# Kernel optimization log

Hardware: AMD Instinct MI355X
Metric: run time of the kernel (lower is better)

Reference implementation:

```python
import jax, jax.numpy as jnp
import numpy as np

N, E, H, NH = 50000, 500000, 128, 8
DH = H // NH


def _bn(x, g, b, eps=1e-5):
    # BatchNorm1d in training mode: biased batch statistics over the node dim
    mu = x.mean(0)
    var = ((x - mu) ** 2).mean(0)
    return (x - mu) * jax.lax.rsqrt(var + eps) * g + b


def setup_inputs() -> dict:
    key = jax.random.key(0)
    ks = jax.random.split(key, 16)
    W = lambda k, shape: jax.random.normal(k, shape, jnp.float32) * 0.02
    return {
        "h": jax.random.normal(ks[0], (N, H), jnp.float32),
        "eattr": jax.random.normal(ks[1], (E, H), jnp.float32),
        "src": jax.random.randint(ks[2], (E,), 0, N, jnp.int32),
        "dst": jax.random.randint(ks[3], (E,), 0, N, jnp.int32),
        "gin_w1": W(ks[4], (H, H)), "gin_b1": jnp.zeros((H,), jnp.float32),
        "gin_w2": W(ks[5], (H, H)), "gin_b2": jnp.zeros((H,), jnp.float32),
        "wq": W(ks[6], (H, H)), "bq": jnp.zeros((H,), jnp.float32),
        "wk": W(ks[7], (H, H)), "bk": jnp.zeros((H,), jnp.float32),
        "wv": W(ks[8], (H, H)), "bv": jnp.zeros((H,), jnp.float32),
        "nl_g": jnp.ones((H,), jnp.float32), "nl_b": jnp.zeros((H,), jnp.float32),
        "na_g": jnp.ones((H,), jnp.float32), "na_b": jnp.zeros((H,), jnp.float32),
        "no_g": jnp.ones((H,), jnp.float32), "no_b": jnp.zeros((H,), jnp.float32),
        "ffn1_w": W(ks[9], (2 * H, H)), "ffn1_b": jnp.zeros((2 * H,), jnp.float32),
        "ffn2_w": W(ks[10], (H, 2 * H)), "ffn2_b": jnp.zeros((H,), jnp.float32),
    }


def reference(h, eattr, src, dst, gin_w1, gin_b1, gin_w2, gin_b2,
              wq, bq, wk, bk, wv, bv, nl_g, nl_b, na_g, na_b, no_g, no_b,
              ffn1_w, ffn1_b, ffn2_w, ffn2_b):
    h_in = h

    # --- local model: GINEConv (eps=0) ---
    msg = jax.nn.relu(h[src] + eattr)                       # [E,H]
    agg = jax.ops.segment_sum(msg, dst, num_segments=N)     # [N,H]
    z = h + agg                                             # (1+eps)*h + sum
    h_local = jax.nn.relu(z @ gin_w1.T + gin_b1) @ gin_w2.T + gin_b2
    h_local = _bn(h_in + h_local, nl_g, nl_b)               # dropout=0

    # --- global attention: SparseMHA over the edge list ---
    scale = DH ** -0.5
    q = ((h @ wq.T + bq) * scale).reshape(N, NH, DH)
    k = (h @ wk.T + bk).reshape(N, NH, DH)
    v = (h @ wv.T + bv).reshape(N, NH, DH)
    s = jnp.einsum("ehd,ehd->eh", q[src], k[dst])           # per-edge scores [E,NH]
    m = jax.ops.segment_max(s, src, num_segments=N)         # row-wise max [N,NH]
    p = jnp.exp(s - m[src])
    denom = jax.ops.segment_sum(p, src, num_segments=N)     # [N,NH]
    attn = p / denom[src]                                   # sparse row softmax [E,NH]
    out = jax.ops.segment_sum(attn[:, :, None] * v[dst], src, num_segments=N)
    h_attn = out.reshape(N, H)
    h_attn = _bn(h_in + h_attn, na_g, na_b)

    # --- combine + FFN + out norm ---
    hc = h_local + h_attn
    hc = hc + (jax.nn.relu(hc @ ffn1_w.T + ffn1_b) @ ffn2_w.T + ffn2_b)
    hc = _bn(hc, no_g, no_b)
    return (hc, eattr)
```

## Files before the change

### kernel.cpp

```cpp
#include <hip/hip_runtime.h>

#define NN 50000
#define NE 500000
#define HD 128

typedef unsigned short ushort_t;
typedef __bf16 bf16x8 __attribute__((ext_vector_type(8)));
typedef float f32x4 __attribute__((ext_vector_type(4)));

static __device__ __forceinline__ unsigned short f2bf(float f) {
  unsigned int u = __float_as_uint(f);
  unsigned int r = (u + 0x7fffu + ((u >> 16) & 1u)) >> 16;
  return (unsigned short)r;
}
static __device__ __forceinline__ float2 ldbf2(const unsigned short* p) {
  unsigned int u = *reinterpret_cast<const unsigned int*>(p);
  return make_float2(__uint_as_float(u << 16), __uint_as_float(u & 0xffff0000u));
}

__global__ __launch_bounds__(256) void hist_kernel(const int* __restrict__ src, const int* __restrict__ dst,
                                                   int* __restrict__ deg_src, int* __restrict__ deg_dst, int E) {
  int e = blockIdx.x * 256 + threadIdx.x;
  if (e < E) {
    atomicAdd(&deg_dst[dst[e]], 1);
    atomicAdd(&deg_src[src[e]], 1);
  }
}

__global__ __launch_bounds__(1024) void scan_kernel(const int* __restrict__ deg_dst, const int* __restrict__ deg_src,
                                                    int* __restrict__ off_dst, int* __restrict__ cur_dst,
                                                    int* __restrict__ off_src, int* __restrict__ cur_src, int N) {
  const int* deg = blockIdx.x ? deg_src : deg_dst;
  int* off = blockIdx.x ? off_src : off_dst;
  int* cur = blockIdx.x ? cur_src : cur_dst;
  const int CH = (N + 1023) / 1024;
  int t = threadIdx.x;
  int base = t * CH;
  int sum = 0;
  for (int i = 0; i < CH; ++i) { int idx = base + i; if (idx < N) sum += deg[idx]; }
  __shared__ int ls[1024];
  ls[t] = sum;
  __syncthreads();
  for (int o = 1; o < 1024; o <<= 1) {
    int u = (t >= o) ? ls[t - o] : 0;
    __syncthreads();
    ls[t] += u;
    __syncthreads();
  }
  int run = ls[t] - sum;
  for (int i = 0; i < CH; ++i) {
    int idx = base + i;
    if (idx < N) { off[idx] = run; cur[idx] = run; run += deg[idx]; }
  }
  if (t == 1023) off[N] = ls[1023];
}

__global__ __launch_bounds__(256) void scatter_kernel(const int* __restrict__ src, const int* __restrict__ dst,
                                                      int* __restrict__ cur_src, int* __restrict__ cur_dst,
                                                      int* __restrict__ eid_src, int* __restrict__ eid_dst, int E) {
  int e = blockIdx.x * 256 + threadIdx.x;
  if (e < E) {
    int p = atomicAdd(&cur_dst[dst[e]], 1); eid_dst[p] = e;
    int q = atomicAdd(&cur_src[src[e]], 1); eid_src[q] = e;
  }
}

__global__ __launch_bounds__(256) void hconv_kernel(const float* __restrict__ h, ushort_t* __restrict__ hb, int total4) {
  int i = blockIdx.x * 256 + threadIdx.x;
  if (i >= total4) return;
  float4 v = reinterpret_cast<const float4*>(h)[i];
  ushort4 u = { f2bf(v.x), f2bf(v.y), f2bf(v.z), f2bf(v.w) };
  reinterpret_cast<ushort4*>(hb)[i] = u;
}

template <int K, int OUTC, int MODE>
__global__ __launch_bounds__(256) void gemm_kernel(const ushort_t* __restrict__ A, const float* __restrict__ W,
                                                   const float* __restrict__ bias, const float* __restrict__ resid,
                                                   void* __restrict__ out, float scale, int nrows) {
  constexpr int KP = K + 8;
  __shared__ __align__(16) ushort_t wlds[OUTC * KP];
  constexpr int NLOAD = OUTC * K / 4;
  for (int idx = threadIdx.x; idx < NLOAD; idx += 256) {
    int r = idx / (K / 4), c4 = idx % (K / 4);
    float4 wv = reinterpret_cast<const float4*>(W)[idx];
    ushort_t* d = &wlds[r * KP + c4 * 4];
    d[0] = f2bf(wv.x); d[1] = f2bf(wv.y); d[2] = f2bf(wv.z); d[3] = f2bf(wv.w);
  }
  __syncthreads();
  const int wave = threadIdx.x >> 6, lane = threadIdx.x & 63;
  const int row0 = (blockIdx.x * 4 + wave) * 16;
  if (row0 >= nrows) return;
  const int m = lane & 15, quad = lane >> 4;
  bf16x8 afrag[K / 32];
  {
    const ushort_t* ar = A + (size_t)(row0 + m) * K + quad * 8;
#pragma unroll
    for (int kk = 0; kk < K / 32; ++kk)
      afrag[kk] = *reinterpret_cast<const bf16x8*>(ar + kk * 32);
  }
  f32x4 acc[OUTC / 16] = {};
#pragma unroll
  for (int c = 0; c < OUTC / 16; ++c) {
    const ushort_t* wr = &wlds[(c * 16 + m) * KP + quad * 8];
#pragma unroll
    for (int kk = 0; kk < K / 32; ++kk) {
      bf16x8 bfrag = *reinterpret_cast<const bf16x8*>(wr + kk * 32);
      acc[c] = __builtin_amdgcn_mfma_f32_16x16x32_bf16(afrag[kk], bfrag, acc[c], 0, 0, 0);
    }
  }
#pragma unroll
  for (int c = 0; c < OUTC / 16; ++c) {
    int col = c * 16 + m;
    float bv = bias[col];
#pragma unroll
    for (int r = 0; r < 4; ++r) {
      int grow = row0 + quad * 4 + r;
      float val = (acc[c][r] + bv) * scale;
      if constexpr (MODE & 1) val = fmaxf(val, 0.0f);
      if constexpr (MODE & 2) val += resid[(size_t)grow * OUTC + col];
      if constexpr (MODE & 4) ((ushort_t*)out)[(size_t)grow * OUTC + col] = f2bf(val);
      else ((float*)out)[(size_t)grow * OUTC + col] = val;
    }
  }
}

__global__ __launch_bounds__(256) void agg_kernel(const float* __restrict__ h, const float* __restrict__ eattr,
                                                  const int* __restrict__ src, const int* __restrict__ off_dst,
                                                  const int* __restrict__ eid_dst, float* __restrict__ out_eattr,
                                                  ushort_t* __restrict__ z_bf, int N) {
  int wave = threadIdx.x >> 6, lane = threadIdx.x & 63;
  int n = blockIdx.x * 4 + wave;
  if (n >= N) return;
  int c2 = lane * 2;
  float a0 = 0.f, a1 = 0.f;
  int beg = off_dst[n], end = off_dst[n + 1];
  for (int i = beg; i < end; ++i) {
    int e = eid_dst[i];
    int s = src[e];
    float2 ea = *reinterpret_cast<const float2*>(eattr + (size_t)e * HD + c2);
    *reinterpret_cast<float2*>(out_eattr + (size_t)e * HD + c2) = ea;
    float2 hs = *reinterpret_cast<const float2*>(h + (size_t)s * HD + c2);
    a0 += fmaxf(hs.x + ea.x, 0.f);
    a1 += fmaxf(hs.y + ea.y, 0.f);
  }
  float2 hn = *reinterpret_cast<const float2*>(h + (size_t)n * HD + c2);
  ushort2 u = { f2bf(hn.x + a0), f2bf(hn.y + a1) };
  *reinterpret_cast<ushort2*>(z_bf + (size_t)n * HD + c2) = u;
}

__global__ __launch_bounds__(256) void attn_kernel(const ushort_t* __restrict__ qb, const ushort_t* __restrict__ kb,
                                                   const ushort_t* __restrict__ vb, const int* __restrict__ off_src,
                                                   const int* __restrict__ eid_src, const int* __restrict__ dst,
                                                   const float* __restrict__ h, float* __restrict__ X2, int N) {
  int wave = threadIdx.x >> 6, lane = threadIdx.x & 63;
  int n = blockIdx.x * 4 + wave;
  if (n >= N) return;
  int c2 = lane * 2;
  float2 qv = ldbf2(qb + (size_t)n * HD + c2);
  float m = -__builtin_inff(), l = 0.f, a0 = 0.f, a1 = 0.f;
  int beg = off_src[n], end = off_src[n + 1];
  for (int i = beg; i < end; ++i) {
    int e = eid_src[i];
    int d = dst[e];
    float2 kd = ldbf2(kb + (size_t)d * HD + c2);
    float s = qv.x * kd.x + qv.y * kd.y;
    s += __shfl_xor(s, 1, 64);
    s += __shfl_xor(s, 2, 64);
    s += __shfl_xor(s, 4, 64);
    float2 vd = ldbf2(vb + (size_t)d * HD + c2);
    float nm = fmaxf(m, s);
    float al = __expf(m - nm);
    float p = __expf(s - nm);
    l = l * al + p;
    a0 = a0 * al + p * vd.x;
    a1 = a1 * al + p * vd.y;
    m = nm;
  }
  float inv = (end > beg) ? 1.0f / l : 0.f;
  size_t base = (size_t)n * HD + c2;
  float2 hv = *reinterpret_cast<const float2*>(h + base);
  float2 o = make_float2(hv.x + a0 * inv, hv.y + a1 * inv);
  *reinterpret_cast<float2*>(X2 + base) = o;
}

__global__ __launch_bounds__(256) void stats_kernel(const float* __restrict__ X, float* __restrict__ sums,
                                                    float* __restrict__ sumsq, int N) {
  int col = threadIdx.x & 127, half = threadIdx.x >> 7;
  float s = 0.f, s2 = 0.f;
  for (int r = blockIdx.x * 2 + half; r < N; r += gridDim.x * 2) {
    float v = X[(size_t)r * HD + col];
    s += v;
    s2 += v * v;
  }
  __shared__ float ls[256], ls2[256];
  ls[threadIdx.x] = s;
  ls2[threadIdx.x] = s2;
  __syncthreads();
  if (half == 0) {
    s += ls[threadIdx.x + 128];
    s2 += ls2[threadIdx.x + 128];
    atomicAdd(&sums[col], s);
    atomicAdd(&sumsq[col], s2);
  }
}

__global__ void coeff_kernel(const float* __restrict__ sums, const float* __restrict__ sumsq,
                             const float* __restrict__ g, const float* __restrict__ b, float* __restrict__ ab, int N) {
  int c = threadIdx.x;
  float inv_n = 1.0f / (float)N;
  float mu = sums[c] * inv_n;
  float var = sumsq[c] * inv_n - mu * mu;
  float a = g[c] * rsqrtf(var + 1e-5f);
  ab[c] = a;
  ab[128 + c] = b[c] - mu * a;
}

__global__ __launch_bounds__(256) void combine_kernel(const float* __restrict__ X1, const float* __restrict__ X2,
                                                      const float* __restrict__ ab1, const float* __restrict__ ab2,
                                                      float* __restrict__ hc_f, ushort_t* __restrict__ hc_b, int total4) {
  int i = blockIdx.x * 256 + threadIdx.x;
  if (i >= total4) return;
  float4 x1 = reinterpret_cast<const float4*>(X1)[i];
  float4 x2 = reinterpret_cast<const float4*>(X2)[i];
  int c = (i * 4) & 127;
  float4 r;
  r.x = x1.x * ab1[c + 0] + ab1[128 + c + 0] + x2.x * ab2[c + 0] + ab2[128 + c + 0];
  r.y = x1.y * ab1[c + 1] + ab1[128 + c + 1] + x2.y * ab2[c + 1] + ab2[128 + c + 1];
  r.z = x1.z * ab1[c + 2] + ab1[128 + c + 2] + x2.z * ab2[c + 2] + ab2[128 + c + 2];
  r.w = x1.w * ab1[c + 3] + ab1[128 + c + 3] + x2.w * ab2[c + 3] + ab2[128 + c + 3];
  reinterpret_cast<float4*>(hc_f)[i] = r;
  ushort4 u = { f2bf(r.x), f2bf(r.y), f2bf(r.z), f2bf(r.w) };
  reinterpret_cast<ushort4*>(hc_b)[i] = u;
}

__global__ __launch_bounds__(256) void final_kernel(const float* __restrict__ X3, const float* __restrict__ ab,
                                                    float* __restrict__ out, int total4) {
  int i = blockIdx.x * 256 + threadIdx.x;
  if (i >= total4) return;
  float4 x = reinterpret_cast<const float4*>(X3)[i];
  int c = (i * 4) & 127;
  float4 r;
  r.x = x.x * ab[c + 0] + ab[128 + c + 0];
  r.y = x.y * ab[c + 1] + ab[128 + c + 1];
  r.z = x.z * ab[c + 2] + ab[128 + c + 2];
  r.w = x.w * ab[c + 3] + ab[128 + c + 3];
  reinterpret_cast<float4*>(out)[i] = r;
}

extern "C" void kernel_launch(void* const* d_in, const int* in_sizes, int n_in,
                              void* d_out, int out_size, void* d_ws, size_t ws_size,
                              hipStream_t stream) {
  const float* h = (const float*)d_in[0];
  const float* eattr = (const float*)d_in[1];
  const int* src = (const int*)d_in[2];
  const int* dst = (const int*)d_in[3];
  const float* gin_w1 = (const float*)d_in[4];
  const float* gin_b1 = (const float*)d_in[5];
  const float* gin_w2 = (const float*)d_in[6];
  const float* gin_b2 = (const float*)d_in[7];
  const float* wq = (const float*)d_in[8];
  const float* bq = (const float*)d_in[9];
  const float* wk = (const float*)d_in[10];
  const float* bk = (const float*)d_in[11];
  const float* wv = (const float*)d_in[12];
  const float* bv = (const float*)d_in[13];
  const float* nl_g = (const float*)d_in[14];
  const float* nl_b = (const float*)d_in[15];
  const float* na_g = (const float*)d_in[16];
  const float* na_b = (const float*)d_in[17];
  const float* no_g = (const float*)d_in[18];
  const float* no_b = (const float*)d_in[19];
  const float* ffn1_w = (const float*)d_in[20];
  const float* ffn1_b = (const float*)d_in[21];
  const float* ffn2_w = (const float*)d_in[22];
  const float* ffn2_b = (const float*)d_in[23];

  const int N = NN, E = NE;
  char* ws = (char*)d_ws;
  size_t off = 0;
  auto alloc = [&](size_t bytes) -> void* {
    void* p = ws + off;
    off += (bytes + 255) & ~(size_t)255;
    return p;
  };

  ushort_t* h_bf = (ushort_t*)alloc((size_t)N * HD * 2);
  ushort_t* q_bf = (ushort_t*)alloc((size_t)N * HD * 2);
  ushort_t* k_bf = (ushort_t*)alloc((size_t)N * HD * 2);
  ushort_t* v_bf = (ushort_t*)alloc((size_t)N * HD * 2);
  ushort_t* z_bf = (ushort_t*)alloc((size_t)N * HD * 2);
  ushort_t* mid1 = (ushort_t*)alloc((size_t)N * HD * 2);
  ushort_t* hc_bf = (ushort_t*)alloc((size_t)N * HD * 2);
  ushort_t* mid2 = (ushort_t*)alloc((size_t)N * 256 * 2);
  float* X1 = (float*)alloc((size_t)N * HD * 4);
  float* X2 = (float*)alloc((size_t)N * HD * 4);
  float* X3 = (float*)alloc((size_t)N * HD * 4);
  float* hc_f = (float*)alloc((size_t)N * HD * 4);
  int* deg_dst = (int*)alloc((size_t)N * 4);
  int* deg_src = (int*)alloc((size_t)N * 4);
  float* stats = (float*)alloc(6 * 128 * 4);
  size_t zero_bytes = (size_t)((char*)(stats + 6 * 128) - (char*)deg_dst);
  int* off_dst = (int*)alloc((size_t)(N + 1) * 4);
  int* off_src = (int*)alloc((size_t)(N + 1) * 4);
  int* cur_dst = (int*)alloc((size_t)N * 4);
  int* cur_src = (int*)alloc((size_t)N * 4);
  int* eid_dst = (int*)alloc((size_t)E * 4);
  int* eid_src = (int*)alloc((size_t)E * 4);
  float* ab1 = (float*)alloc(256 * 4);
  float* ab2 = (float*)alloc(256 * 4);
  float* ab3 = (float*)alloc(256 * 4);

  float* sums1 = stats, *sq1 = stats + 128;
  float* sums2 = stats + 256, *sq2 = stats + 384;
  float* sums3 = stats + 512, *sq3 = stats + 640;

  float* out_hc = (float*)d_out;
  float* out_eattr = (float*)d_out + (size_t)N * HD;

  hipMemsetAsync(deg_dst, 0, zero_bytes, stream);

  const int egrid = (E + 255) / 256;
  hist_kernel<<<egrid, 256, 0, stream>>>(src, dst, deg_src, deg_dst, E);
  scan_kernel<<<2, 1024, 0, stream>>>(deg_dst, deg_src, off_dst, cur_dst, off_src, cur_src, N);
  scatter_kernel<<<egrid, 256, 0, stream>>>(src, dst, cur_src, cur_dst, eid_src, eid_dst, E);

  const int total4 = N * HD / 4;
  const int cgrid = (total4 + 255) / 256;
  hconv_kernel<<<cgrid, 256, 0, stream>>>(h, h_bf, total4);

  const int ggrid = (N / 16 + 3) / 4;
  const float scale = 0.25f;
  gemm_kernel<128, 128, 4><<<ggrid, 256, 0, stream>>>(h_bf, wq, bq, nullptr, q_bf, scale, N);
  gemm_kernel<128, 128, 4><<<ggrid, 256, 0, stream>>>(h_bf, wk, bk, nullptr, k_bf, 1.0f, N);
  gemm_kernel<128, 128, 4><<<ggrid, 256, 0, stream>>>(h_bf, wv, bv, nullptr, v_bf, 1.0f, N);

  agg_kernel<<<N / 4, 256, 0, stream>>>(h, eattr, src, off_dst, eid_dst, out_eattr, z_bf, N);
  gemm_kernel<128, 128, 5><<<ggrid, 256, 0, stream>>>(z_bf, gin_w1, gin_b1, nullptr, mid1, 1.0f, N);
  gemm_kernel<128, 128, 2><<<ggrid, 256, 0, stream>>>(mid1, gin_w2, gin_b2, h, X1, 1.0f, N);

  attn_kernel<<<N / 4, 256, 0, stream>>>(q_bf, k_bf, v_bf, off_src, eid_src, dst, h, X2, N);

  stats_kernel<<<256, 256, 0, stream>>>(X1, sums1, sq1, N);
  stats_kernel<<<256, 256, 0, stream>>>(X2, sums2, sq2, N);
  coeff_kernel<<<1, 128, 0, stream>>>(sums1, sq1, nl_g, nl_b, ab1, N);
  coeff_kernel<<<1, 128, 0, stream>>>(sums2, sq2, na_g, na_b, ab2, N);
  combine_kernel<<<cgrid, 256, 0, stream>>>(X1, X2, ab1, ab2, hc_f, hc_bf, total4);

  gemm_kernel<128, 256, 5><<<ggrid, 256, 0, stream>>>(hc_bf, ffn1_w, ffn1_b, nullptr, mid2, 1.0f, N);
  gemm_kernel<256, 128, 2><<<ggrid, 256, 0, stream>>>(mid2, ffn2_w, ffn2_b, hc_f, X3, 1.0f, N);

  stats_kernel<<<256, 256, 0, stream>>>(X3, sums3, sq3, N);
  coeff_kernel<<<1, 128, 0, stream>>>(sums3, sq3, no_g, no_b, ab3, N);
  final_kernel<<<cgrid, 256, 0, stream>>>(X3, ab3, out_hc, total4);
}
```

Baseline: 1.131 ms.

## Store neighbor ids in CSR, unroll gather loops by four with prefetch

The scatter step now writes the neighbor index itself (and the edge id with the source for dst-CSR), which removes one dependent indirect load per edge in the aggregation and attention kernels. Both loops are unrolled by four, with the next group of indices prefetched, so more independent gathers are in flight per wave. Edge-attribute reads and copies use nontemporal hints to avoid polluting the cache. In exchange the dst pair array doubles in size and the kernels use more registers.

```diff
diff --git a/kernel.cpp b/kernel.cpp
--- a/kernel.cpp
+++ b/kernel.cpp
@@ -7,6 +7,7 @@
 typedef unsigned short ushort_t;
 typedef __bf16 bf16x8 __attribute__((ext_vector_type(8)));
 typedef float f32x4 __attribute__((ext_vector_type(4)));
+typedef float f32x2 __attribute__((ext_vector_type(2)));
 
 static __device__ __forceinline__ unsigned short f2bf(float f) {
   unsigned int u = __float_as_uint(f);
@@ -57,11 +58,12 @@
 
 __global__ __launch_bounds__(256) void scatter_kernel(const int* __restrict__ src, const int* __restrict__ dst,
                                                       int* __restrict__ cur_src, int* __restrict__ cur_dst,
-                                                      int* __restrict__ eid_src, int* __restrict__ eid_dst, int E) {
+                                                      int* __restrict__ adj_src, int2* __restrict__ pair_dst, int E) {
   int e = blockIdx.x * 256 + threadIdx.x;
   if (e < E) {
-    int p = atomicAdd(&cur_dst[dst[e]], 1); eid_dst[p] = e;
-    int q = atomicAdd(&cur_src[src[e]], 1); eid_src[q] = e;
+    int s = src[e], d = dst[e];
+    int p = atomicAdd(&cur_dst[d], 1); pair_dst[p] = make_int2(e, s);
+    int q = atomicAdd(&cur_src[s], 1); adj_src[q] = d;
   }
 }
 
@@ -125,21 +127,48 @@
 }
 
 __global__ __launch_bounds__(256) void agg_kernel(const float* __restrict__ h, const float* __restrict__ eattr,
-                                                  const int* __restrict__ src, const int* __restrict__ off_dst,
-                                                  const int* __restrict__ eid_dst, float* __restrict__ out_eattr,
-                                                  ushort_t* __restrict__ z_bf, int N) {
+                                                  const int* __restrict__ off_dst, const int2* __restrict__ pair_dst,
+                                                  float* __restrict__ out_eattr, ushort_t* __restrict__ z_bf, int N) {
   int wave = threadIdx.x >> 6, lane = threadIdx.x & 63;
   int n = blockIdx.x * 4 + wave;
   if (n >= N) return;
   int c2 = lane * 2;
   float a0 = 0.f, a1 = 0.f;
   int beg = off_dst[n], end = off_dst[n + 1];
-  for (int i = beg; i < end; ++i) {
-    int e = eid_dst[i];
-    int s = src[e];
-    float2 ea = *reinterpret_cast<const float2*>(eattr + (size_t)e * HD + c2);
-    *reinterpret_cast<float2*>(out_eattr + (size_t)e * HD + c2) = ea;
-    float2 hs = *reinterpret_cast<const float2*>(h + (size_t)s * HD + c2);
+  int i = beg;
+  int mainend = beg + ((end - beg) & ~3);
+  if (i < mainend) {
+    int2 p0 = pair_dst[i], p1 = pair_dst[i + 1], p2 = pair_dst[i + 2], p3 = pair_dst[i + 3];
+    for (;;) {
+      f32x2 ea0 = __builtin_nontemporal_load(reinterpret_cast<const f32x2*>(eattr + (size_t)p0.x * HD + c2));
+      f32x2 ea1 = __builtin_nontemporal_load(reinterpret_cast<const f32x2*>(eattr + (size_t)p1.x * HD + c2));
+      f32x2 ea2 = __builtin_nontemporal_load(reinterpret_cast<const f32x2*>(eattr + (size_t)p2.x * HD + c2));
+      f32x2 ea3 = __builtin_nontemporal_load(reinterpret_cast<const f32x2*>(eattr + (size_t)p3.x * HD + c2));
+      f32x2 hs0 = *reinterpret_cast<const f32x2*>(h + (size_t)p0.y * HD + c2);
+      f32x2 hs1 = *reinterpret_cast<const f32x2*>(h + (size_t)p1.y * HD + c2);
+      f32x2 hs2 = *reinterpret_cast<const f32x2*>(h + (size_t)p2.y * HD + c2);
+      f32x2 hs3 = *reinterpret_cast<const f32x2*>(h + (size_t)p3.y * HD + c2);
+      int ni = i + 4;
+      int pi = (ni < mainend) ? ni : beg;
+      int2 q0 = pair_dst[pi], q1 = pair_dst[pi + 1], q2 = pair_dst[pi + 2], q3 = pair_dst[pi + 3];
+      __builtin_nontemporal_store(ea0, reinterpret_cast<f32x2*>(out_eattr + (size_t)p0.x * HD + c2));
+      __builtin_nontemporal_store(ea1, reinterpret_cast<f32x2*>(out_eattr + (size_t)p1.x * HD + c2));
+      __builtin_nontemporal_store(ea2, reinterpret_cast<f32x2*>(out_eattr + (size_t)p2.x * HD + c2));
+      __builtin_nontemporal_store(ea3, reinterpret_cast<f32x2*>(out_eattr + (size_t)p3.x * HD + c2));
+      a0 += (fmaxf(hs0.x + ea0.x, 0.f) + fmaxf(hs1.x + ea1.x, 0.f)) +
+            (fmaxf(hs2.x + ea2.x, 0.f) + fmaxf(hs3.x + ea3.x, 0.f));
+      a1 += (fmaxf(hs0.y + ea0.y, 0.f) + fmaxf(hs1.y + ea1.y, 0.f)) +
+            (fmaxf(hs2.y + ea2.y, 0.f) + fmaxf(hs3.y + ea3.y, 0.f));
+      p0 = q0; p1 = q1; p2 = q2; p3 = q3;
+      i = ni;
+      if (i >= mainend) break;
+    }
+  }
+  for (; i < end; ++i) {
+    int2 p = pair_dst[i];
+    f32x2 ea = __builtin_nontemporal_load(reinterpret_cast<const f32x2*>(eattr + (size_t)p.x * HD + c2));
+    f32x2 hs = *reinterpret_cast<const f32x2*>(h + (size_t)p.y * HD + c2);
+    __builtin_nontemporal_store(ea, reinterpret_cast<f32x2*>(out_eattr + (size_t)p.x * HD + c2));
     a0 += fmaxf(hs.x + ea.x, 0.f);
     a1 += fmaxf(hs.y + ea.y, 0.f);
   }
@@ -150,7 +179,7 @@
 
 __global__ __launch_bounds__(256) void attn_kernel(const ushort_t* __restrict__ qb, const ushort_t* __restrict__ kb,
                                                    const ushort_t* __restrict__ vb, const int* __restrict__ off_src,
-                                                   const int* __restrict__ eid_src, const int* __restrict__ dst,
+                                                   const int* __restrict__ adj_src,
                                                    const float* __restrict__ h, float* __restrict__ X2, int N) {
   int wave = threadIdx.x >> 6, lane = threadIdx.x & 63;
   int n = blockIdx.x * 4 + wave;
@@ -159,9 +188,45 @@
   float2 qv = ldbf2(qb + (size_t)n * HD + c2);
   float m = -__builtin_inff(), l = 0.f, a0 = 0.f, a1 = 0.f;
   int beg = off_src[n], end = off_src[n + 1];
-  for (int i = beg; i < end; ++i) {
-    int e = eid_src[i];
-    int d = dst[e];
+  int i = beg;
+  int mainend = beg + ((end - beg) & ~3);
+  if (i < mainend) {
+    int d0 = adj_src[i], d1 = adj_src[i + 1], d2 = adj_src[i + 2], d3 = adj_src[i + 3];
+    for (;;) {
+      float2 k0 = ldbf2(kb + (size_t)d0 * HD + c2);
+      float2 k1 = ldbf2(kb + (size_t)d1 * HD + c2);
+      float2 k2 = ldbf2(kb + (size_t)d2 * HD + c2);
+      float2 k3 = ldbf2(kb + (size_t)d3 * HD + c2);
+      float2 v0 = ldbf2(vb + (size_t)d0 * HD + c2);
+      float2 v1 = ldbf2(vb + (size_t)d1 * HD + c2);
+      float2 v2 = ldbf2(vb + (size_t)d2 * HD + c2);
+      float2 v3 = ldbf2(vb + (size_t)d3 * HD + c2);
+      int ni = i + 4;
+      int pi = (ni < mainend) ? ni : beg;
+      int e0 = adj_src[pi], e1 = adj_src[pi + 1], e2 = adj_src[pi + 2], e3 = adj_src[pi + 3];
+      float s0 = qv.x * k0.x + qv.y * k0.y;
+      float s1 = qv.x * k1.x + qv.y * k1.y;
+      float s2 = qv.x * k2.x + qv.y * k2.y;
+      float s3 = qv.x * k3.x + qv.y * k3.y;
+      s0 += __shfl_xor(s0, 1, 64); s0 += __shfl_xor(s0, 2, 64); s0 += __shfl_xor(s0, 4, 64);
+      s1 += __shfl_xor(s1, 1, 64); s1 += __shfl_xor(s1, 2, 64); s1 += __shfl_xor(s1, 4, 64);
+      s2 += __shfl_xor(s2, 1, 64); s2 += __shfl_xor(s2, 2, 64); s2 += __shfl_xor(s2, 4, 64);
+      s3 += __shfl_xor(s3, 1, 64); s3 += __shfl_xor(s3, 2, 64); s3 += __shfl_xor(s3, 4, 64);
+      float smax = fmaxf(fmaxf(s0, s1), fmaxf(s2, s3));
+      float nm = fmaxf(m, smax);
+      float al = __expf(m - nm);
+      float p0 = __expf(s0 - nm), p1 = __expf(s1 - nm), p2 = __expf(s2 - nm), p3 = __expf(s3 - nm);
+      l = l * al + ((p0 + p1) + (p2 + p3));
+      a0 = a0 * al + ((p0 * v0.x + p1 * v1.x) + (p2 * v2.x + p3 * v3.x));
+      a1 = a1 * al + ((p0 * v0.y + p1 * v1.y) + (p2 * v2.y + p3 * v3.y));
+      m = nm;
+      d0 = e0; d1 = e1; d2 = e2; d3 = e3;
+      i = ni;
+      if (i >= mainend) break;
+    }
+  }
+  for (; i < end; ++i) {
+    int d = adj_src[i];
     float2 kd = ldbf2(kb + (size_t)d * HD + c2);
     float s = qv.x * kd.x + qv.y * kd.y;
     s += __shfl_xor(s, 1, 64);
@@ -304,8 +369,8 @@
   int* off_src = (int*)alloc((size_t)(N + 1) * 4);
   int* cur_dst = (int*)alloc((size_t)N * 4);
   int* cur_src = (int*)alloc((size_t)N * 4);
-  int* eid_dst = (int*)alloc((size_t)E * 4);
-  int* eid_src = (int*)alloc((size_t)E * 4);
+  int2* pair_dst = (int2*)alloc((size_t)E * 8);
+  int* adj_src = (int*)alloc((size_t)E * 4);
   float* ab1 = (float*)alloc(256 * 4);
   float* ab2 = (float*)alloc(256 * 4);
   float* ab3 = (float*)alloc(256 * 4);
@@ -322,7 +387,7 @@
   const int egrid = (E + 255) / 256;
   hist_kernel<<<egrid, 256, 0, stream>>>(src, dst, deg_src, deg_dst, E);
   scan_kernel<<<2, 1024, 0, stream>>>(deg_dst, deg_src, off_dst, cur_dst, off_src, cur_src, N);
-  scatter_kernel<<<egrid, 256, 0, stream>>>(src, dst, cur_src, cur_dst, eid_src, eid_dst, E);
+  scatter_kernel<<<egrid, 256, 0, stream>>>(src, dst, cur_src, cur_dst, adj_src, pair_dst, E);
 
   const int total4 = N * HD / 4;
   const int cgrid = (total4 + 255) / 256;
@@ -334,11 +399,11 @@
   gemm_kernel<128, 128, 4><<<ggrid, 256, 0, stream>>>(h_bf, wk, bk, nullptr, k_bf, 1.0f, N);
   gemm_kernel<128, 128, 4><<<ggrid, 256, 0, stream>>>(h_bf, wv, bv, nullptr, v_bf, 1.0f, N);
 
-  agg_kernel<<<N / 4, 256, 0, stream>>>(h, eattr, src, off_dst, eid_dst, out_eattr, z_bf, N);
+  agg_kernel<<<N / 4, 256, 0, stream>>>(h, eattr, off_dst, pair_dst, out_eattr, z_bf, N);
   gemm_kernel<128, 128, 5><<<ggrid, 256, 0, stream>>>(z_bf, gin_w1, gin_b1, nullptr, mid1, 1.0f, N);
   gemm_kernel<128, 128, 2><<<ggrid, 256, 0, stream>>>(mid1, gin_w2, gin_b2, h, X1, 1.0f, N);
 
-  attn_kernel<<<N / 4, 256, 0, stream>>>(q_bf, k_bf, v_bf, off_src, eid_src, dst, h, X2, N);
+  attn_kernel<<<N / 4, 256, 0, stream>>>(q_bf, k_bf, v_bf, off_src, adj_src, h, X2, N);
 
   stats_kernel<<<256, 256, 0, stream>>>(X1, sums1, sq1, N);
   stats_kernel<<<256, 256, 0, stream>>>(X2, sums2, sq2, N);
```

Result: faster. 1.003 ms (-11.3%).
